# Kernel tuning notes

Hardware: AMD Instinct MI355X
Metric: run time of the kernel (lower is better)

The kernel has to match this reference:

```python
import jax, jax.numpy as jnp
import numpy as np

N_NODES = 50000
N_EDGES = 800000
D_IN = 512
D_OUT = 128


def setup_inputs() -> dict:
    key = jax.random.key(0)
    k1, k2, k3, k4, k5 = jax.random.split(key, 5)
    x = jax.random.normal(k1, (N_NODES, D_IN), dtype=jnp.float32)
    edge_src = jax.random.randint(k2, (N_EDGES,), 0, N_NODES, dtype=jnp.int32)
    edge_dst = jnp.sort(jax.random.randint(k3, (N_EDGES,), 0, N_NODES, dtype=jnp.int32))
    edge_val = jax.random.uniform(k4, (N_EDGES,), dtype=jnp.float32)
    stdv = 1.0 / np.sqrt(D_OUT)
    weight = jax.random.uniform(k5, (D_IN, D_OUT), dtype=jnp.float32,
                                minval=-stdv, maxval=stdv)
    return {"x": x, "edge_src": edge_src, "edge_dst": edge_dst,
            "edge_val": edge_val, "weight": weight}


def reference(x, edge_src, edge_dst, edge_val, weight):
    # support = X @ W : dense GEMM [N, D_in] x [D_in, D_out]
    support = x @ weight
    # output = A @ support : SpMM via gather + weighted segment-sum over dst
    gathered = support[edge_src] * edge_val[:, None]  # [E, D_out]
    output = jax.ops.segment_sum(gathered, edge_dst, num_segments=x.shape[0])
    return output
```

## Files before the change

### kernel.cpp

```cpp
#include <hip/hip_runtime.h>
#include <hip/hip_bf16.h>

#define M_NODES 50000
#define K_DIM   512
#define N_DIM   128

typedef short s16x8 __attribute__((ext_vector_type(8)));
typedef float f32x4 __attribute__((ext_vector_type(4)));

static __device__ __forceinline__ ushort f2bf(float f) {
  uint u = __float_as_uint(f);
  u += 0x7fff + ((u >> 16) & 1);
  return (ushort)(u >> 16);
}

static __device__ __forceinline__ uint cvtpk(float lo, float hi) {
  uint r;
  asm("v_cvt_pk_bf16_f32 %0, %1, %2" : "=v"(r) : "v"(lo), "v"(hi));
  return r;
}

static __device__ __forceinline__ void g2l16(const void* g, void* l) {
  __builtin_amdgcn_global_load_lds((const __attribute__((address_space(1))) void*)g,
                                   (__attribute__((address_space(3))) void*)l, 16, 0, 0);
}

__global__ __launch_bounds__(256) void prep_zero(const float* __restrict__ W,
                                                 ushort* __restrict__ Wt,
                                                 float4* __restrict__ o4, int n4) {
  const int t = blockIdx.x * 256 + threadIdx.x;
  const int stride = gridDim.x * 256;
  for (int i = t; i < n4; i += stride) o4[i] = make_float4(0.f, 0.f, 0.f, 0.f);
  if (t < 16384) {
    int k  = t >> 5;
    int c0 = (t & 31) * 4;
    float4 v = *reinterpret_cast<const float4*>(&W[(size_t)k * N_DIM + c0]);
    Wt[(size_t)(c0 + 0) * K_DIM + k] = f2bf(v.x);
    Wt[(size_t)(c0 + 1) * K_DIM + k] = f2bf(v.y);
    Wt[(size_t)(c0 + 2) * K_DIM + k] = f2bf(v.z);
    Wt[(size_t)(c0 + 3) * K_DIM + k] = f2bf(v.w);
  }
}

#define GBK 32
#define NKS (K_DIM / GBK)

__global__ __launch_bounds__(256, 4) void gemm_mfma(const float* __restrict__ X,
                                                    const ushort* __restrict__ Wt,
                                                    float* __restrict__ S) {
  __shared__ float  Albs[2][64 * 32];
  __shared__ ushort Blbs[2][128 * 32];

  const int tid = threadIdx.x;
  const int w   = tid >> 6;
  const int l   = tid & 63;
  const int l15 = l & 15, lg = l >> 4;
  const int wr  = w >> 1, wc = w & 1;
  const int row0 = blockIdx.x * 64;

  const float* aSrc[2];
#pragma unroll
  for (int i = 0; i < 2; ++i) {
    int q = i * 256 + w * 64 + l;
    int r = q >> 3;
    int c = (q & 7) ^ (r & 7);
    int rg = row0 + r; if (rg >= M_NODES) rg = M_NODES - 1;
    aSrc[i] = X + (size_t)rg * K_DIM + c * 4;
  }
  const ushort* bSrc[2];
#pragma unroll
  for (int i = 0; i < 2; ++i) {
    int q = i * 256 + w * 64 + l;
    int col = q >> 2, j = q & 3;
    bSrc[i] = Wt + (size_t)col * K_DIM + j * 8;
  }

  f32x4 acc[2][4];
#pragma unroll
  for (int am = 0; am < 2; ++am)
#pragma unroll
    for (int bn = 0; bn < 4; ++bn) acc[am][bn] = (f32x4){0.f, 0.f, 0.f, 0.f};

#define STAGE(buf, kk) { \
  _Pragma("unroll") for (int i = 0; i < 2; ++i) \
    g2l16(aSrc[i] + (kk), (char*)&Albs[buf][0] + (size_t)(i * 256 + w * 64) * 16); \
  _Pragma("unroll") for (int i = 0; i < 2; ++i) \
    g2l16(bSrc[i] + (kk), (char*)&Blbs[buf][0] + (size_t)(i * 256 + w * 64) * 16); }

#define COMPUTE(buf) { \
  s16x8 af[2], bfr[4]; \
  _Pragma("unroll") for (int am = 0; am < 2; ++am) { \
    const int r = wr * 32 + am * 16 + l15; \
    const int s = r & 7; \
    float4 f0 = *reinterpret_cast<const float4*>(&Albs[buf][(r * 8 + ((lg * 2) ^ s)) * 4]); \
    float4 f1 = *reinterpret_cast<const float4*>(&Albs[buf][(r * 8 + ((lg * 2 + 1) ^ s)) * 4]); \
    union { s16x8 v; uint u[4]; } a; \
    a.u[0] = cvtpk(f0.x, f0.y); a.u[1] = cvtpk(f0.z, f0.w); \
    a.u[2] = cvtpk(f1.x, f1.y); a.u[3] = cvtpk(f1.z, f1.w); \
    af[am] = a.v; } \
  _Pragma("unroll") for (int bn = 0; bn < 4; ++bn) { \
    const int c = wc * 64 + bn * 16 + l15; \
    bfr[bn] = *reinterpret_cast<const s16x8*>(&Blbs[buf][c * 32 + lg * 8]); } \
  _Pragma("unroll") for (int am = 0; am < 2; ++am) \
    _Pragma("unroll") for (int bn = 0; bn < 4; ++bn) \
      acc[am][bn] = __builtin_amdgcn_mfma_f32_16x16x32_bf16(af[am], bfr[bn], acc[am][bn], 0, 0, 0); }

  STAGE(0, 0)
  __syncthreads();
#pragma unroll
  for (int t = 0; t < NKS; ++t) {
    if (t + 1 < NKS) STAGE((t + 1) & 1, (t + 1) * GBK)
    COMPUTE(t & 1)
    __syncthreads();
  }
#undef STAGE
#undef COMPUTE

#pragma unroll
  for (int am = 0; am < 2; ++am) {
#pragma unroll
    for (int rr = 0; rr < 4; ++rr) {
      const int row = row0 + wr * 32 + am * 16 + lg * 4 + rr;
      if (row < M_NODES) {
        float* sp = S + (size_t)row * N_DIM + wc * 64 + l15;
#pragma unroll
        for (int bn = 0; bn < 4; ++bn)
          sp[bn * 16] = acc[am][bn][rr];
      }
    }
  }
}

#define EPB 256
#define CHUNK 64
#define SB 8

__global__ __launch_bounds__(128, 4) void spmm_edges(const float* __restrict__ S,
                                                     const int* __restrict__ esrc,
                                                     const int* __restrict__ edst,
                                                     const float* __restrict__ eval,
                                                     float* __restrict__ out) {
  __shared__ int   s_src[EPB];
  __shared__ int   s_dst[EPB];
  __shared__ float s_val[EPB];

  const int e0  = blockIdx.x * EPB;
  const int tid = threadIdx.x;

#pragma unroll
  for (int i = 0; i < EPB / 128; ++i) {
    int idx = tid + i * 128;
    s_src[idx] = esrc[e0 + idx];
    s_dst[idx] = edst[e0 + idx];
    s_val[idx] = eval[e0 + idx];
  }
  __syncthreads();

  const int wid  = tid >> 6;
  const int l    = tid & 63;
  const int half = (wid << 1) | (l >> 5);
  const int hl   = l & 31;
  const int base = half * CHUNK;
  const int c0   = hl * 4;

  const int first = s_dst[base];
  int   cur = first;
  f32x4 acc = {0.f, 0.f, 0.f, 0.f};

  f32x4 bufA[SB], bufB[SB];

#define SLOAD(BUF, B) { \
  _Pragma("unroll") for (int j = 0; j < SB; ++j) \
    BUF[j] = *reinterpret_cast<const f32x4*>( \
        S + (size_t)s_src[base + (B) * SB + j] * N_DIM + c0); \
  __builtin_amdgcn_sched_barrier(0); }

#define FLUSH() { \
  float* op = out + (size_t)cur * N_DIM + c0; \
  if (cur == first) { \
    atomicAdd(op + 0, acc[0]); atomicAdd(op + 1, acc[1]); \
    atomicAdd(op + 2, acc[2]); atomicAdd(op + 3, acc[3]); \
  } else { \
    *reinterpret_cast<f32x4*>(op) = acc; \
  } \
  acc = (f32x4){0.f, 0.f, 0.f, 0.f}; }

#define SPROC(BUF, B) { \
  _Pragma("unroll") for (int j = 0; j < SB; ++j) { \
    const int e = base + (B) * SB + j; \
    const int d = s_dst[e]; \
    if (d != cur) { FLUSH() cur = d; } \
    const float vv = s_val[e]; \
    acc[0] += vv * BUF[j][0]; acc[1] += vv * BUF[j][1]; \
    acc[2] += vv * BUF[j][2]; acc[3] += vv * BUF[j][3]; } }

  SLOAD(bufA, 0)
#pragma unroll
  for (int b = 0; b < CHUNK / SB; b += 2) {
    if (b + 1 < CHUNK / SB) SLOAD(bufB, b + 1)
    SPROC(bufA, b)
    if (b + 2 < CHUNK / SB) SLOAD(bufA, b + 2)
    SPROC(bufB, b + 1)
  }
  {
    float* op = out + (size_t)cur * N_DIM + c0;
    atomicAdd(op + 0, acc[0]); atomicAdd(op + 1, acc[1]);
    atomicAdd(op + 2, acc[2]); atomicAdd(op + 3, acc[3]);
  }
#undef SLOAD
#undef SPROC
#undef FLUSH
}

extern "C" void kernel_launch(void* const* d_in, const int* in_sizes, int n_in,
                              void* d_out, int out_size, void* d_ws, size_t ws_size,
                              hipStream_t stream) {
  const float* x        = (const float*)d_in[0];
  const int*   edge_src = (const int*)d_in[1];
  const int*   edge_dst = (const int*)d_in[2];
  const float* edge_val = (const float*)d_in[3];
  const float* weight   = (const float*)d_in[4];
  float*       out      = (float*)d_out;

  float*  support = (float*)d_ws;
  ushort* wt      = (ushort*)((char*)d_ws + (size_t)M_NODES * N_DIM * 4);

  const int n_edges = in_sizes[1];

  prep_zero<<<dim3(512), dim3(256), 0, stream>>>(weight, wt, (float4*)d_out,
                                                 out_size / 4);

  gemm_mfma<<<dim3((M_NODES + 63) / 64), dim3(256), 0, stream>>>(x, wt, support);

  spmm_edges<<<dim3(n_edges / EPB), dim3(128), 0, stream>>>(support, edge_src,
                                                            edge_dst, edge_val, out);
}
```

Measured before the change: 251.0 us.

## Store GEMM support matrix in bf16 and gather bf16 rows in SpMM

The GEMM epilogue now writes the intermediate support matrix as bf16 instead of fp32, which halves its write traffic and the gather traffic of the edge kernel. The SpMM is remapped so each wave handles 128 consecutive edges with 64 lanes each owning two columns (one 32-bit load per edge), and the prefetch depth rises to 32 edges per stage. This adds one more rounding step on the intermediate, which lowers accuracy, and the larger register buffers may reduce occupancy.

```diff
diff --git a/kernel.cpp b/kernel.cpp
--- a/kernel.cpp
+++ b/kernel.cpp
@@ -47,7 +47,7 @@
 
 __global__ __launch_bounds__(256, 4) void gemm_mfma(const float* __restrict__ X,
                                                     const ushort* __restrict__ Wt,
-                                                    float* __restrict__ S) {
+                                                    ushort* __restrict__ Sb) {
   __shared__ float  Albs[2][64 * 32];
   __shared__ ushort Blbs[2][128 * 32];
 
@@ -122,20 +122,20 @@
     for (int rr = 0; rr < 4; ++rr) {
       const int row = row0 + wr * 32 + am * 16 + lg * 4 + rr;
       if (row < M_NODES) {
-        float* sp = S + (size_t)row * N_DIM + wc * 64 + l15;
+        ushort* sp = Sb + (size_t)row * N_DIM + wc * 64 + l15;
 #pragma unroll
         for (int bn = 0; bn < 4; ++bn)
-          sp[bn * 16] = acc[am][bn][rr];
+          sp[bn * 16] = f2bf(acc[am][bn][rr]);
       }
     }
   }
 }
 
 #define EPB 256
-#define CHUNK 64
-#define SB 8
-
-__global__ __launch_bounds__(128, 4) void spmm_edges(const float* __restrict__ S,
+#define CPW 128
+#define SB 32
+
+__global__ __launch_bounds__(128, 4) void spmm_edges(const ushort* __restrict__ Sb,
                                                      const int* __restrict__ esrc,
                                                      const int* __restrict__ edst,
                                                      const float* __restrict__ eval,
@@ -156,34 +156,27 @@
   }
   __syncthreads();
 
-  const int wid  = tid >> 6;
+  const int w    = tid >> 6;
   const int l    = tid & 63;
-  const int half = (wid << 1) | (l >> 5);
-  const int hl   = l & 31;
-  const int base = half * CHUNK;
-  const int c0   = hl * 4;
+  const int base = w * CPW;
+  const uint colb = (uint)l * 4u;
 
   const int first = s_dst[base];
   int   cur = first;
-  f32x4 acc = {0.f, 0.f, 0.f, 0.f};
-
-  f32x4 bufA[SB], bufB[SB];
+  float ax = 0.f, ay = 0.f;
+
+  uint bufA[SB], bufB[SB];
 
 #define SLOAD(BUF, B) { \
   _Pragma("unroll") for (int j = 0; j < SB; ++j) \
-    BUF[j] = *reinterpret_cast<const f32x4*>( \
-        S + (size_t)s_src[base + (B) * SB + j] * N_DIM + c0); \
-  __builtin_amdgcn_sched_barrier(0); }
+    BUF[j] = *reinterpret_cast<const uint*>( \
+        (const char*)Sb + (size_t)s_src[base + (B) * SB + j] * 256 + colb); }
 
 #define FLUSH() { \
-  float* op = out + (size_t)cur * N_DIM + c0; \
-  if (cur == first) { \
-    atomicAdd(op + 0, acc[0]); atomicAdd(op + 1, acc[1]); \
-    atomicAdd(op + 2, acc[2]); atomicAdd(op + 3, acc[3]); \
-  } else { \
-    *reinterpret_cast<f32x4*>(op) = acc; \
-  } \
-  acc = (f32x4){0.f, 0.f, 0.f, 0.f}; }
+  float* op = out + (size_t)cur * N_DIM + l * 2; \
+  if (cur == first) { atomicAdd(op, ax); atomicAdd(op + 1, ay); } \
+  else { *reinterpret_cast<float2*>(op) = make_float2(ax, ay); } \
+  ax = 0.f; ay = 0.f; }
 
 #define SPROC(BUF, B) { \
   _Pragma("unroll") for (int j = 0; j < SB; ++j) { \
@@ -191,21 +184,21 @@
     const int d = s_dst[e]; \
     if (d != cur) { FLUSH() cur = d; } \
     const float vv = s_val[e]; \
-    acc[0] += vv * BUF[j][0]; acc[1] += vv * BUF[j][1]; \
-    acc[2] += vv * BUF[j][2]; acc[3] += vv * BUF[j][3]; } }
+    const float lo = __uint_as_float(BUF[j] << 16); \
+    const float hi = __uint_as_float(BUF[j] & 0xffff0000u); \
+    ax += vv * lo; ay += vv * hi; } }
 
   SLOAD(bufA, 0)
 #pragma unroll
-  for (int b = 0; b < CHUNK / SB; b += 2) {
-    if (b + 1 < CHUNK / SB) SLOAD(bufB, b + 1)
+  for (int b = 0; b < CPW / SB; b += 2) {
+    if (b + 1 < CPW / SB) SLOAD(bufB, b + 1)
     SPROC(bufA, b)
-    if (b + 2 < CHUNK / SB) SLOAD(bufA, b + 2)
+    if (b + 2 < CPW / SB) SLOAD(bufA, b + 2)
     SPROC(bufB, b + 1)
   }
   {
-    float* op = out + (size_t)cur * N_DIM + c0;
-    atomicAdd(op + 0, acc[0]); atomicAdd(op + 1, acc[1]);
-    atomicAdd(op + 2, acc[2]); atomicAdd(op + 3, acc[3]);
+    float* op = out + (size_t)cur * N_DIM + l * 2;
+    atomicAdd(op, ax); atomicAdd(op + 1, ay);
   }
 #undef SLOAD
 #undef SPROC
@@ -222,16 +215,16 @@
   const float* weight   = (const float*)d_in[4];
   float*       out      = (float*)d_out;
 
-  float*  support = (float*)d_ws;
-  ushort* wt      = (ushort*)((char*)d_ws + (size_t)M_NODES * N_DIM * 4);
+  ushort* sb = (ushort*)d_ws;
+  ushort* wt = (ushort*)((char*)d_ws + (size_t)M_NODES * N_DIM * 2);
 
   const int n_edges = in_sizes[1];
 
   prep_zero<<<dim3(512), dim3(256), 0, stream>>>(weight, wt, (float4*)d_out,
                                                  out_size / 4);
 
-  gemm_mfma<<<dim3((M_NODES + 63) / 64), dim3(256), 0, stream>>>(x, wt, support);
-
-  spmm_edges<<<dim3(n_edges / EPB), dim3(128), 0, stream>>>(support, edge_src,
+  gemm_mfma<<<dim3((M_NODES + 63) / 64), dim3(256), 0, stream>>>(x, wt, sb);
+
+  spmm_edges<<<dim3(n_edges / EPB), dim3(128), 0, stream>>>(sb, edge_src,
                                                             edge_dst, edge_val, out);
 }
```

Result: faster. 214.1 us (-14.7%).
